# Kernel tuning notes

Measured on AMD Instinct MI355X. Metric: run time of the kernel, lower is better.

Reference implementation:

```python
import jax, jax.numpy as jnp
import numpy as np

HEADS = 8
EPS = 1e-12  # F.normalize default eps


def conv1x1(t, w):
    # t: (B, Cin, H, W); w: (Cout, Cin) -> (B, Cout, H, W)
    return jnp.einsum('bchw,oc->bohw', t, w)


def cosine_attn(q, k, v, scale):
    # q: (B,h,d,Nq); k,v: (B,h,d,Nk). Cosine attention: L2-normalize over feature dim d.
    q = q / jnp.maximum(jnp.linalg.norm(q, axis=2, keepdims=True), EPS)
    k = k / jnp.maximum(jnp.linalg.norm(k, axis=2, keepdims=True), EPS)
    attn = jnp.einsum('bhdq,bhdk->bhqk', q, k) * scale
    attn = jax.nn.softmax(attn, axis=-1)
    return jnp.einsum('bhqk,bhdk->bhdq', attn, v)  # (B,h,d,Nq)


def setup_inputs() -> dict:
    key = jax.random.key(0)
    ks = jax.random.split(key, 8)
    B, C, H, W, L = 8, 512, 64, 64, 16
    def w(k, o, i):
        return jax.random.normal(k, (o, i), dtype=jnp.float32) * (1.0 / np.sqrt(i))
    return {
        'x': jax.random.normal(ks[0], (B, C, H, W), dtype=jnp.float32),
        'latents': jax.random.normal(ks[1], (1, C, 1, L), dtype=jnp.float32) * 0.02,
        'w_q_lat': w(ks[2], C, C),
        'w_kv_x': w(ks[3], 2 * C, C),
        'w_q_x': w(ks[4], C, C),
        'w_kv_lat': w(ks[5], 2 * C, C),
        'w_proj': w(ks[6], C, C),
        'b_proj': jnp.zeros((C,), dtype=jnp.float32),
    }


def reference(x, latents, w_q_lat, w_kv_x, w_q_x, w_kv_lat, w_proj, b_proj):
    B, C, H, W = x.shape
    L = latents.shape[-1]
    h = HEADS
    d = C // h
    scale = d ** (-0.5)

    # latents read from spatial features (compression)
    lat = jnp.broadcast_to(latents, (B, C, 1, L))
    ql = conv1x1(lat, w_q_lat).reshape(B, h, d, L)
    kvx = conv1x1(x, w_kv_x)
    kx = kvx[:, :C].reshape(B, h, d, H * W)
    vx = kvx[:, C:].reshape(B, h, d, H * W)
    lat_read = cosine_attn(ql, kx, vx, scale).reshape(B, C, 1, L)

    # latents write back into features (expansion)
    qx = conv1x1(x, w_q_x).reshape(B, h, d, H * W)
    kvl = conv1x1(lat_read, w_kv_lat)
    kl = kvl[:, :C].reshape(B, h, d, L)
    vl = kvl[:, C:].reshape(B, h, d, L)
    x_write = cosine_attn(qx, kl, vl, scale).reshape(B, C, H, W)

    # output projection (dropout p=0 -> identity)
    return conv1x1(x_write, w_proj) + b_proj[None, :, None, None]
```

## Files before the change

kernel.cpp:

```cpp
#include <hip/hip_runtime.h>


typedef __bf16 bf16x8 __attribute__((ext_vector_type(8)));
typedef float floatx4 __attribute__((ext_vector_type(4)));
typedef short short8_t __attribute__((ext_vector_type(8)));
typedef short short4_t __attribute__((ext_vector_type(4)));

#define DEV __device__ __forceinline__

DEV float bf2f(unsigned short u){ union{unsigned int i; float f;} v; v.i = ((unsigned int)u)<<16; return v.f; }
DEV unsigned short f2bf(float f){
  __bf16 h = (__bf16)f;
  unsigned short u; __builtin_memcpy(&u, &h, 2); return u;
}

DEV void glds16(const void* g, void* l){
  __builtin_amdgcn_global_load_lds((const __attribute__((address_space(1))) void*)g,
                                   (__attribute__((address_space(3))) void*)l, 16, 0, 0);
}

#define OFF_XT     256ull
#define OFF_KVX    (OFF_XT + 33554432ull)
#define OFF_WKVX   (OFF_KVX + 67108864ull)
#define OFF_WQX    (OFF_WKVX + 1048576ull)
#define OFF_WKVL   (OFF_WQX + 524288ull)
#define OFF_WPROJ  (OFF_WKVL + 1048576ull)
#define OFF_WQLAT  (OFF_WPROJ + 524288ull)
#define OFF_LATF   (OFF_WQLAT + 524288ull)
#define OFF_BIAS   (OFF_LATF + 32768ull)
#define OFF_QLH    (OFF_BIAS + 4096ull)
#define OFF_GNUM   (OFF_QLH + 32768ull)
#define OFF_GDEN   (OFF_GNUM + 524288ull)
#define OFF_KVL    (OFF_GDEN + 4096ull)
#define OFF_KHAT   (OFF_KVL + 524288ull)
#define OFF_GVL    (OFF_KHAT + 524288ull)

__global__ void k_sniff(const unsigned short* __restrict__ x, int* flag){
  int t = threadIdx.x;
  int m = 0;
  for (int i = t; i < 4096; i += 256){ int e = (x[i]>>7)&0xFF; m = (e>m)?e:m; }
  __shared__ int red[256];
  red[t] = m; __syncthreads();
  for (int s = 128; s > 0; s >>= 1){ if (t < s) red[t] = (red[t+s]>red[t])?red[t+s]:red[t]; __syncthreads(); }
  if (t == 0) flag[0] = (red[0] > 150) ? 1 : 0;
}

__global__ __launch_bounds__(256) void k_prep(const void* s0, const void* s1, const void* s2,
                                              const void* s3, const void* s4,
                                              const void* slat, const void* sbias,
                                              unsigned short* __restrict__ wdst,
                                              float* __restrict__ latf, float* __restrict__ biasf,
                                              const int* __restrict__ flag){
  int b = blockIdx.x, t = threadIdx.x;
  int isf = *flag;
  if (b < 896){
    int e = b*2048 + t*8;
    const void* src; int off;
    if (e < 524288)      { src = s0; off = e; }
    else if (e < 786432) { src = s1; off = e - 524288; }
    else if (e < 1310720){ src = s2; off = e - 786432; }
    else if (e < 1572864){ src = s3; off = e - 1310720; }
    else                 { src = s4; off = e - 1572864; }
    if (isf){
      const float* s = (const float*)src + off;
      float4 v0 = *(const float4*)(s);
      float4 v1 = *(const float4*)(s+4);
      unsigned short tmp[8] __attribute__((aligned(16)));
      tmp[0]=f2bf(v0.x); tmp[1]=f2bf(v0.y); tmp[2]=f2bf(v0.z); tmp[3]=f2bf(v0.w);
      tmp[4]=f2bf(v1.x); tmp[5]=f2bf(v1.y); tmp[6]=f2bf(v1.z); tmp[7]=f2bf(v1.w);
      *(short8_t*)&wdst[e] = *(short8_t*)tmp;
    } else {
      *(short8_t*)&wdst[e] = *(const short8_t*)((const unsigned short*)src + off);
    }
  } else if (b < 900){
    int i = (b-896)*2048 + t*8;
#pragma unroll
    for (int j = 0; j < 8; ++j)
      latf[i+j] = isf ? ((const float*)slat)[i+j] : bf2f(((const unsigned short*)slat)[i+j]);
  } else {
    if (t < 512) biasf[t] = isf ? ((const float*)sbias)[t] : bf2f(((const unsigned short*)sbias)[t]);
  }
}

__global__ __launch_bounds__(256) void k_xt(const void* __restrict__ xraw, unsigned short* __restrict__ xT,
                                            const int* __restrict__ flag){
  int nb = blockIdx.x, cb = blockIdx.y, b = blockIdx.z;
  int n0 = nb*64, c0 = cb*64;
  __shared__ unsigned short tile[64][72];
  int t = threadIdx.x;
  if (*flag){
    const float* xp = (const float*)xraw;
#pragma unroll
    for (int i = 0; i < 4; ++i){
      int ch = i*256 + t; int c = ch>>4, n4 = (ch&15)*4;
      float4 v = *(const float4*)&xp[((size_t)(b*512 + c0 + c))*4096 + n0 + n4];
      int cc = n4 ^ (((c>>3)&7)<<3);
      tile[c][cc+0]=f2bf(v.x); tile[c][cc+1]=f2bf(v.y); tile[c][cc+2]=f2bf(v.z); tile[c][cc+3]=f2bf(v.w);
    }
  } else {
    const unsigned short* xp = (const unsigned short*)xraw;
#pragma unroll
    for (int i = 0; i < 2; ++i){
      int ch = i*256 + t; int c = ch>>3, n8 = (ch&7)*8;
      *(short8_t*)&tile[c][n8 ^ (((c>>3)&7)<<3)] =
        *(const short8_t*)&xp[((size_t)(b*512 + c0 + c))*4096 + n0 + n8];
    }
  }
  __syncthreads();
#pragma unroll
  for (int i = 0; i < 2; ++i){
    int ch = i*256 + t; int n = ch>>3, c8 = (ch&7)*8;
    unsigned short tmp[8] __attribute__((aligned(16)));
#pragma unroll
    for (int j = 0; j < 8; ++j){
      int c = c8 + j;
      tmp[j] = tile[c][n ^ (((c>>3)&7)<<3)];
    }
    *(short8_t*)&xT[((size_t)(b*4096 + n0 + n))*512 + c0 + c8] = *(short8_t*)tmp;
  }
}

__global__ __launch_bounds__(256) void k_ql(const unsigned short* __restrict__ wqlat,
                                            const float* __restrict__ latf, float* __restrict__ qlh){
  int h = blockIdx.x, o0 = h*64;
  extern __shared__ char smr[];
  float* latb = (float*)smr;
  unsigned short* wt = (unsigned short*)(smr + 8192);
  float* qbuf = (float*)(smr + 8192 + 17408);
  float* rinv = (float*)(smr + 8192 + 17408 + 4096);
  int t = threadIdx.x;
  int o = t>>2, l4 = (t&3)*4;
  float acc[4] = {0.f,0.f,0.f,0.f};
  for (int kk = 0; kk < 512; kk += 128){
    __syncthreads();
#pragma unroll
    for (int j = 0; j < 8; ++j){ int i = j*256 + t; latb[i] = latf[kk*16 + i]; }
#pragma unroll
    for (int j = 0; j < 4; ++j){ int ch = j*256 + t; int r = ch>>4, kc = (ch&15)*8;
      *(short8_t*)&wt[r*136 + kc] = *(const short8_t*)&wqlat[(size_t)(o0+r)*512 + kk + kc]; }
    __syncthreads();
    for (int k = 0; k < 128; ++k){
      float w = bf2f(wt[o*136 + k]);
      const float* lr = &latb[k*16 + l4];
#pragma unroll
      for (int j = 0; j < 4; ++j) acc[j] += w*lr[j];
    }
  }
#pragma unroll
  for (int j = 0; j < 4; ++j) qbuf[o*16 + l4 + j] = acc[j];
  __syncthreads();
  if (t < 16){
    float ss = 0.f;
    for (int oo = 0; oo < 64; ++oo){ float v = qbuf[oo*16 + t]; ss += v*v; }
    rinv[t] = 0.125f / fmaxf(sqrtf(ss), 1e-12f);
  }
  __syncthreads();
#pragma unroll
  for (int j = 0; j < 4; ++j) qlh[(h*16 + l4 + j)*64 + o] = acc[j]*rinv[l4 + j];
}

DEV void stage_ab(const unsigned short* __restrict__ Ap0, const unsigned short* __restrict__ Ap1,
                  const unsigned short* __restrict__ Bp, int kk,
                  unsigned short* At, unsigned short* Bt, int wave, int rsub, int koff){
#pragma unroll
  for (int c2 = 0; c2 < 4; ++c2){
    int chunk = wave*4 + c2;
    int row = chunk*8 + rsub;
    const unsigned short* gp = (chunk < 8) ? (Ap0 + (size_t)row*512 + kk + koff)
                                           : (Ap1 + (size_t)(row-64)*512 + kk + koff);
    glds16(gp, At + chunk*512);
  }
#pragma unroll
  for (int c2 = 0; c2 < 4; ++c2){
    int chunk = wave*4 + c2;
    int row = chunk*8 + rsub;
    glds16(Bp + (size_t)row*512 + kk + koff, Bt + chunk*512);
  }
}

DEV void gemm128_db(const unsigned short* __restrict__ Ap0, const unsigned short* __restrict__ Ap1,
                    const unsigned short* __restrict__ Bp,
                    char* smr, floatx4 (&acc)[4][4]){
  unsigned short* At0 = (unsigned short*)smr;
  unsigned short* Bt0 = (unsigned short*)(smr + 16384);
  unsigned short* At1 = (unsigned short*)(smr + 32768);
  unsigned short* Bt1 = (unsigned short*)(smr + 49152);
  int t = threadIdx.x, lane = t&63, wave = t>>6;
  int wm = wave>>1, wn = wave&1, lr = lane&15, lq = lane>>4;
  int rsub = lane>>3;
  int koff = ((lane&7) ^ rsub)*8;
  int sw = lr&7;
  stage_ab(Ap0, Ap1, Bp, 0, At0, Bt0, wave, rsub, koff);
  __syncthreads();
  for (int kk = 0; kk < 512; kk += 64){
    int cur = (kk>>6)&1;
    unsigned short* Ac = cur ? At1 : At0;
    unsigned short* Bc = cur ? Bt1 : Bt0;
    if (kk < 448){
      stage_ab(Ap0, Ap1, Bp, kk+64, cur ? At0 : At1, cur ? Bt0 : Bt1, wave, rsub, koff);
    }
    __builtin_amdgcn_s_setprio(1);
#pragma unroll
    for (int ks = 0; ks < 2; ++ks){
      int vo = ((ks*4 + lq) ^ sw)*8;
      bf16x8 a[4], b[4];
#pragma unroll
      for (int mt = 0; mt < 4; ++mt) a[mt] = *(const bf16x8*)&Ac[(wm*64 + mt*16 + lr)*64 + vo];
#pragma unroll
      for (int nt = 0; nt < 4; ++nt) b[nt] = *(const bf16x8*)&Bc[(wn*64 + nt*16 + lr)*64 + vo];
#pragma unroll
      for (int mt = 0; mt < 4; ++mt)
#pragma unroll
        for (int nt = 0; nt < 4; ++nt)
          acc[mt][nt] = __builtin_amdgcn_mfma_f32_16x16x32_bf16(a[mt], b[nt], acc[mt][nt], 0, 0, 0);
    }
    __builtin_amdgcn_s_setprio(0);
    __syncthreads();
  }
}

__global__ __launch_bounds__(256) void k_kvattn1(const unsigned short* __restrict__ wkvx,
                                                 const unsigned short* __restrict__ xT,
                                                 const float* __restrict__ qlh2,
                                                 float* __restrict__ gnum, float* __restrict__ gden){
  int nb = blockIdx.x, h = blockIdx.y, b = blockIdx.z;
  int n0 = nb*128;
  extern __shared__ char smr[];
  unsigned short* kt  = (unsigned short*)smr;
  unsigned short* vt  = (unsigned short*)(smr + 18432);
  unsigned short* pt  = (unsigned short*)(smr + 35840);
  unsigned short* qls = (unsigned short*)(smr + 65536);
  float* ssq  = (float*)(smr + 67840);
  float* wred = (float*)(smr + 68352);
  int t = threadIdx.x, lane = t&63, wave = t>>6;
  int wm = wave>>1, wn = wave&1, lr = lane&15, lq = lane>>4;
  for (int i = t; i < 1024; i += 256) qls[(i>>6)*72 + (i&63)] = f2bf(qlh2[(size_t)h*1024 + i]);
  floatx4 acc[4][4];
  floatx4 zero = {0.f,0.f,0.f,0.f};
#pragma unroll
  for (int i = 0; i < 4; ++i) for (int j = 0; j < 4; ++j) acc[i][j] = zero;
  gemm128_db(wkvx + (size_t)(h*64)*512, wkvx + (size_t)(512 + h*64)*512,
             xT + ((size_t)(b*4096 + n0))*512, smr, acc);
  if (wm == 0){
#pragma unroll
    for (int nt = 0; nt < 4; ++nt){
      float s = 0.f;
#pragma unroll
      for (int mt = 0; mt < 4; ++mt)
#pragma unroll
        for (int r = 0; r < 4; ++r) s += acc[mt][nt][r]*acc[mt][nt][r];
      s += __shfl_xor(s, 16); s += __shfl_xor(s, 32);
      if (lq == 0) ssq[wn*64 + nt*16 + lr] = 1.f / fmaxf(sqrtf(s), 1e-12f);
    }
  } else {
#pragma unroll
    for (int mt = 0; mt < 4; ++mt)
#pragma unroll
      for (int nt = 0; nt < 4; ++nt){
        int col = wn*64 + nt*16 + lr;
#pragma unroll
        for (int r = 0; r < 4; ++r) vt[(mt*16 + lq*4 + r)*136 + col] = f2bf(acc[mt][nt][r]);
      }
  }
  __syncthreads();
  if (wm == 0){
#pragma unroll
    for (int nt = 0; nt < 4; ++nt){
      int col = wn*64 + nt*16 + lr;
      float rinv = ssq[col];
#pragma unroll
      for (int mt = 0; mt < 4; ++mt){
        unsigned short tmp[4] __attribute__((aligned(8)));
#pragma unroll
        for (int r = 0; r < 4; ++r) tmp[r] = f2bf(acc[mt][nt][r]*rinv);
        *(short4_t*)&kt[col*72 + mt*16 + lq*4] = *(short4_t*)tmp;
      }
    }
  }
  __syncthreads();
  floatx4 sl[2]; sl[0] = zero; sl[1] = zero;
#pragma unroll
  for (int ks = 0; ks < 2; ++ks){
    bf16x8 bb = *(const bf16x8*)&qls[lr*72 + ks*32 + lq*8];
#pragma unroll
    for (int i = 0; i < 2; ++i){
      bf16x8 aa = *(const bf16x8*)&kt[((wave*2 + i)*16 + lr)*72 + ks*32 + lq*8];
      sl[i] = __builtin_amdgcn_mfma_f32_16x16x32_bf16(aa, bb, sl[i], 0, 0, 0);
    }
  }
  float dp = 0.f;
  float pv[2][4];
#pragma unroll
  for (int i = 0; i < 2; ++i)
#pragma unroll
    for (int r = 0; r < 4; ++r){ float p = __expf(sl[i][r]); pv[i][r] = p; dp += p; }
  dp += __shfl_xor(dp, 16); dp += __shfl_xor(dp, 32);
  if (lq == 0) wred[wave*16 + lr] = dp;
#pragma unroll
  for (int i = 0; i < 2; ++i){
    unsigned short tmp[4] __attribute__((aligned(8)));
#pragma unroll
    for (int r = 0; r < 4; ++r) tmp[r] = f2bf(pv[i][r]);
    *(short4_t*)&pt[lr*136 + (wave*2 + i)*16 + lq*4] = *(short4_t*)tmp;
  }
  __syncthreads();
  int bh = b*8 + h;
  if (t < 16) atomicAdd(&gden[bh*16 + t], wred[t] + wred[16+t] + wred[32+t] + wred[48+t]);
  floatx4 nacc = zero;
#pragma unroll
  for (int ks = 0; ks < 4; ++ks){
    bf16x8 aa = *(const bf16x8*)&vt[(wave*16 + lr)*136 + ks*32 + lq*8];
    bf16x8 bb = *(const bf16x8*)&pt[lr*136 + ks*32 + lq*8];
    nacc = __builtin_amdgcn_mfma_f32_16x16x32_bf16(aa, bb, nacc, 0, 0, 0);
  }
  float* gp = &gnum[((size_t)bh*16 + lr)*64 + wave*16 + lq*4];
#pragma unroll
  for (int r = 0; r < 4; ++r) atomicAdd(&gp[r], nacc[r]);
}

__global__ __launch_bounds__(256) void k_kvl(const unsigned short* __restrict__ wkvl,
                                             const float* __restrict__ gnum, const float* __restrict__ gden,
                                             float* __restrict__ kvl){
  int ob = blockIdx.x, b = blockIdx.y;
  extern __shared__ char smr[];
  float* latb = (float*)smr;
  unsigned short* wt = (unsigned short*)(smr + 32768);
  int t = threadIdx.x;
  for (int i = t; i < 8192; i += 256){
    int c = i>>4, l = i&15;
    int h = c>>6, d = c&63;
    int bh = b*8 + h;
    latb[i] = gnum[((size_t)(bh*16 + l))*64 + d] / gden[bh*16 + l];
  }
  int o = t>>4, l = t&15;
  int o0 = ob*16;
  float acc = 0.f;
  for (int kk = 0; kk < 512; kk += 128){
    __syncthreads();
    { int r = t>>4, kc = (t&15)*8;
      *(short8_t*)&wt[r*136 + kc] = *(const short8_t*)&wkvl[(size_t)(o0+r)*512 + kk + kc]; }
    __syncthreads();
    for (int k = 0; k < 128; ++k) acc += bf2f(wt[o*136 + k]) * latb[(kk+k)*16 + l];
  }
  kvl[((size_t)(b*1024 + o0 + o))*16 + l] = acc;
}

__global__ void k_klnorm(const float* __restrict__ kvl, float* __restrict__ khat, float* __restrict__ gvl){
  int l = blockIdx.x, h = blockIdx.y, b = blockIdx.z, d = threadIdx.x;
  float kl = kvl[((size_t)(b*1024 + h*64 + d))*16 + l];
  float vl = kvl[((size_t)(b*1024 + 512 + h*64 + d))*16 + l];
  float ss = kl*kl;
  for (int off = 32; off; off >>= 1) ss += __shfl_xor(ss, off);
  float inv = 0.125f / fmaxf(sqrtf(ss), 1e-12f);
  size_t o = ((size_t)((b*8+h)*16 + l))*64 + d;
  khat[o] = kl*inv;
  gvl[o] = vl;
}

__global__ __launch_bounds__(256) void k_mmat(const unsigned short* __restrict__ wproj,
                                              const float* __restrict__ gvl,
                                              unsigned short* __restrict__ Mg){
  int cb = blockIdx.x, h = blockIdx.y, b = blockIdx.z;
  __shared__ unsigned short wt[128*68];
  int t = threadIdx.x;
#pragma unroll
  for (int i = 0; i < 4; ++i){ int ch = i*256 + t; int c = ch>>3, d8 = (ch&7)*8;
    *(short8_t*)&wt[c*68 + d8] = *(const short8_t*)&wproj[(size_t)(cb*128 + c)*512 + h*64 + d8]; }
  int l = t&15, cq = t>>4;
  float v[64];
  const float* vp = &gvl[((size_t)(b*8+h)*16 + l)*64];
#pragma unroll
  for (int j = 0; j < 16; ++j){ float4 f = *(const float4*)&vp[j*4];
    v[j*4+0]=f.x; v[j*4+1]=f.y; v[j*4+2]=f.z; v[j*4+3]=f.w; }
  __syncthreads();
#pragma unroll
  for (int c8 = 0; c8 < 8; ++c8){
    int c = cq*8 + c8;
    float dot = 0.f;
#pragma unroll
    for (int d = 0; d < 64; ++d) dot += bf2f(wt[c*68 + d]) * v[d];
    Mg[((size_t)(b*512) + cb*128 + c)*128 + h*16 + l] = f2bf(dot);
  }
}

__global__ __launch_bounds__(256) void k_attn2p2(const unsigned short* __restrict__ wqx,
                                                 const unsigned short* __restrict__ xT,
                                                 const float* __restrict__ khatg,
                                                 unsigned short* __restrict__ Pg){
  int nb = blockIdx.x, hp = blockIdx.y, b = blockIdx.z;
  int n0 = nb*128;
  extern __shared__ char smr[];
  unsigned short* qt0 = (unsigned short*)smr;
  unsigned short* qt1 = (unsigned short*)(smr + 18432);
  unsigned short* khs = (unsigned short*)(smr + 65536);
  float* ssq = (float*)(smr + 70144);
  int t = threadIdx.x, lane = t&63, wave = t>>6;
  int wm = wave>>1, wn = wave&1, lr = lane&15, lq = lane>>4;
  for (int i = t; i < 2048; i += 256){
    int hh = i>>10, rem = i&1023;
    khs[hh*1152 + (rem>>6)*72 + (rem&63)] = f2bf(khatg[((size_t)(b*8 + hp*2 + hh))*1024 + rem]);
  }
  floatx4 acc[4][4];
  floatx4 zero = {0.f,0.f,0.f,0.f};
#pragma unroll
  for (int i = 0; i < 4; ++i) for (int j = 0; j < 4; ++j) acc[i][j] = zero;
  gemm128_db(wqx + (size_t)(hp*128)*512, wqx + (size_t)(hp*128 + 64)*512,
             xT + ((size_t)(b*4096 + n0))*512, smr, acc);
#pragma unroll
  for (int nt = 0; nt < 4; ++nt){
    float s = 0.f;
#pragma unroll
    for (int mt = 0; mt < 4; ++mt)
#pragma unroll
      for (int r = 0; r < 4; ++r) s += acc[mt][nt][r]*acc[mt][nt][r];
    s += __shfl_xor(s, 16); s += __shfl_xor(s, 32);
    if (lq == 0) ssq[wm*128 + wn*64 + nt*16 + lr] = 1.f / fmaxf(sqrtf(s), 1e-12f);
  }
  __syncthreads();
  unsigned short* qtr = wm ? qt1 : qt0;
#pragma unroll
  for (int nt = 0; nt < 4; ++nt){
    int col = wn*64 + nt*16 + lr;
    float rinv = ssq[wm*128 + col];
#pragma unroll
    for (int mt = 0; mt < 4; ++mt){
      unsigned short tmp[4] __attribute__((aligned(8)));
#pragma unroll
      for (int r = 0; r < 4; ++r) tmp[r] = f2bf(acc[mt][nt][r]*rinv);
      *(short4_t*)&qtr[col*72 + mt*16 + lq*4] = *(short4_t*)tmp;
    }
  }
  __syncthreads();
  floatx4 sl[4];
#pragma unroll
  for (int i = 0; i < 4; ++i) sl[i] = zero;
  unsigned short* qsrc = wm ? qt1 : qt0;
#pragma unroll
  for (int ks = 0; ks < 2; ++ks){
    bf16x8 bb = *(const bf16x8*)&khs[wm*1152 + lr*72 + ks*32 + lq*8];
#pragma unroll
    for (int i = 0; i < 4; ++i){
      bf16x8 aa = *(const bf16x8*)&qsrc[((wn*4 + i)*16 + lr)*72 + ks*32 + lq*8];
      sl[i] = __builtin_amdgcn_mfma_f32_16x16x32_bf16(aa, bb, sl[i], 0, 0, 0);
    }
  }
  int h = hp*2 + wm;
#pragma unroll
  for (int i = 0; i < 4; ++i){
    float p[4], s[4];
#pragma unroll
    for (int r = 0; r < 4; ++r){ p[r] = __expf(sl[i][r]); s[r] = p[r]; }
#pragma unroll
    for (int r = 0; r < 4; ++r){
      s[r] += __shfl_xor(s[r], 1);
      s[r] += __shfl_xor(s[r], 2);
      s[r] += __shfl_xor(s[r], 4);
      s[r] += __shfl_xor(s[r], 8);
    }
    int nbase = wn*64 + i*16 + lq*4;
#pragma unroll
    for (int r = 0; r < 4; ++r)
      Pg[((size_t)(b*4096 + n0 + nbase + r))*128 + h*16 + lr] = f2bf(p[r]/s[r]);
  }
}

__global__ __launch_bounds__(256) void k_out(const unsigned short* __restrict__ Mg,
                                             const unsigned short* __restrict__ Pg,
                                             const float* __restrict__ biasf,
                                             void* __restrict__ outv, const int* __restrict__ flag){
  int nb = blockIdx.x, cb = blockIdx.y, b = blockIdx.z;
  int n0 = nb*128, c0 = cb*64;
  extern __shared__ char smr[];
  unsigned short* At = (unsigned short*)smr;
  unsigned short* Bt = At + 64*136;
  int t = threadIdx.x, lane = t&63, wave = t>>6;
  int wm = wave>>1, wn = wave&1, lr = lane&15, lq = lane>>4;
#pragma unroll
  for (int i = 0; i < 4; ++i){ int ch = i*256 + t; int r = ch>>4, p8 = (ch&15)*8;
    *(short8_t*)&At[r*136 + p8] = *(const short8_t*)&Mg[((size_t)(b*512 + c0 + r))*128 + p8]; }
#pragma unroll
  for (int i = 0; i < 8; ++i){ int ch = i*256 + t; int r = ch>>4, p8 = (ch&15)*8;
    *(short8_t*)&Bt[r*136 + p8] = *(const short8_t*)&Pg[((size_t)(b*4096 + n0 + r))*128 + p8]; }
  __syncthreads();
  floatx4 acc[2][4];
  floatx4 zero = {0.f,0.f,0.f,0.f};
#pragma unroll
  for (int i = 0; i < 2; ++i) for (int j = 0; j < 4; ++j) acc[i][j] = zero;
#pragma unroll
  for (int ks = 0; ks < 4; ++ks){
    bf16x8 a0 = *(const bf16x8*)&At[(wm*32 + lr)*136 + ks*32 + lq*8];
    bf16x8 a1 = *(const bf16x8*)&At[(wm*32 + 16 + lr)*136 + ks*32 + lq*8];
#pragma unroll
    for (int nt = 0; nt < 4; ++nt){
      bf16x8 bb = *(const bf16x8*)&Bt[(wn*64 + nt*16 + lr)*136 + ks*32 + lq*8];
      acc[0][nt] = __builtin_amdgcn_mfma_f32_16x16x32_bf16(a0, bb, acc[0][nt], 0, 0, 0);
      acc[1][nt] = __builtin_amdgcn_mfma_f32_16x16x32_bf16(a1, bb, acc[1][nt], 0, 0, 0);
    }
  }
  __syncthreads();
  float* ct = (float*)smr;
#pragma unroll
  for (int mt = 0; mt < 2; ++mt)
#pragma unroll
    for (int nt = 0; nt < 4; ++nt)
#pragma unroll
      for (int r = 0; r < 4; ++r){
        int row = wm*32 + mt*16 + lq*4 + r;
        ct[row*132 + wn*64 + nt*16 + lr] = acc[mt][nt][r] + biasf[c0 + row];
      }
  __syncthreads();
  if (*flag){
    float* of = (float*)outv;
#pragma unroll
    for (int i = 0; i < 8; ++i){ int ch = i*256 + t; int r = ch>>5, c4 = (ch&31)*4;
      *(float4*)&of[((size_t)(b*512 + c0 + r))*4096 + n0 + c4] = *(float4*)&ct[r*132 + c4]; }
  } else {
    unsigned short* ob = (unsigned short*)outv;
#pragma unroll
    for (int i = 0; i < 4; ++i){ int ch = i*256 + t; int r = ch>>4, c8 = (ch&15)*8;
      unsigned short tmp[8] __attribute__((aligned(16)));
#pragma unroll
      for (int j = 0; j < 8; ++j) tmp[j] = f2bf(ct[r*132 + c8 + j]);
      *(short8_t*)&ob[((size_t)(b*512 + c0 + r))*4096 + n0 + c8] = *(short8_t*)tmp; }
  }
}

extern "C" void kernel_launch(void* const* d_in, const int* in_sizes, int n_in,
                              void* d_out, int out_size, void* d_ws, size_t ws_size,
                              hipStream_t stream){
  (void)in_sizes; (void)n_in; (void)out_size; (void)ws_size;
  char* ws = (char*)d_ws;
  int* flag              = (int*)ws;
  unsigned short* xT     = (unsigned short*)(ws + OFF_XT);
  unsigned short* Pg     = (unsigned short*)(ws + OFF_KVX);
  unsigned short* Mg     = (unsigned short*)(ws + OFF_KVX + 8388608ull);
  unsigned short* wkvx   = (unsigned short*)(ws + OFF_WKVX);
  unsigned short* wqx    = (unsigned short*)(ws + OFF_WQX);
  unsigned short* wkvl   = (unsigned short*)(ws + OFF_WKVL);
  unsigned short* wproj  = (unsigned short*)(ws + OFF_WPROJ);
  float* latf  = (float*)(ws + OFF_LATF);
  float* biasf = (float*)(ws + OFF_BIAS);
  float* qlh   = (float*)(ws + OFF_QLH);
  float* gnum  = (float*)(ws + OFF_GNUM);
  float* gden  = (float*)(ws + OFF_GDEN);
  float* kvl   = (float*)(ws + OFF_KVL);
  float* khat  = (float*)(ws + OFF_KHAT);
  float* gvl   = (float*)(ws + OFF_GVL);

  k_sniff<<<1, 256, 0, stream>>>((const unsigned short*)d_in[0], flag);

  k_prep<<<901, 256, 0, stream>>>(d_in[3], d_in[4], d_in[5], d_in[6], d_in[2],
                                  d_in[1], d_in[7], wkvx, latf, biasf, flag);

  k_xt<<<dim3(64, 8, 8), 256, 0, stream>>>(d_in[0], xT, flag);

  k_ql<<<8, 256, 8192 + 17408 + 4096 + 64, stream>>>((unsigned short*)(ws + OFF_WQLAT), latf, qlh);

  hipMemsetAsync(ws + OFF_GNUM, 0, 524288 + 4096, stream);

  k_kvattn1<<<dim3(32, 8, 8), 256, 68608, stream>>>(wkvx, xT, qlh, gnum, gden);
  k_kvl<<<dim3(64, 8), 256, 32768 + 16*136*2, stream>>>(wkvl, gnum, gden, kvl);
  k_klnorm<<<dim3(16, 8, 8), 64, 0, stream>>>(kvl, khat, gvl);
  k_mmat<<<dim3(4, 8, 8), 256, 0, stream>>>(wproj, gvl, Mg);
  k_attn2p2<<<dim3(32, 4, 8), 256, 71168, stream>>>(wqx, xT, khat, Pg);
  k_out<<<dim3(32, 8, 8), 256, 52224, stream>>>(Mg, Pg, biasf, d_out, flag);
}
```

Measured before the change: 281.7 us.

## Merge prep kernels into one launch and fuse latent kv, norm and proj-matrix kernels

Folds the x transpose, weight conversion, bias conversion, latent-query projection and the memset of the accumulators into a single heterogeneous kernel dispatched by block index. The per-head kv projection, k normalization and proj-weight folding are fused into one kernel per (head, batch). This removes several launches and intermediate global buffers, trading them for fewer, larger blocks in the fused latent stage (only 64 blocks) and a large-shared-memory mega kernel that may lower occupancy for the transpose blocks.

```diff
diff --git a/kernel.cpp b/kernel.cpp
--- a/kernel.cpp
+++ b/kernel.cpp
@@ -45,16 +45,57 @@
   if (t == 0) flag[0] = (red[0] > 150) ? 1 : 0;
 }
 
-__global__ __launch_bounds__(256) void k_prep(const void* s0, const void* s1, const void* s2,
-                                              const void* s3, const void* s4,
-                                              const void* slat, const void* sbias,
-                                              unsigned short* __restrict__ wdst,
-                                              float* __restrict__ latf, float* __restrict__ biasf,
-                                              const int* __restrict__ flag){
-  int b = blockIdx.x, t = threadIdx.x;
+__global__ __launch_bounds__(256) void k_mega1(const void* __restrict__ xraw,
+                                               const void* __restrict__ slat,
+                                               const void* __restrict__ swqlat,
+                                               const void* s0, const void* s1, const void* s2,
+                                               const void* s3, const void* s4,
+                                               const void* __restrict__ sbias,
+                                               unsigned short* __restrict__ xT,
+                                               unsigned short* __restrict__ wdst,
+                                               float* __restrict__ biasf,
+                                               float* __restrict__ qlh,
+                                               float* __restrict__ zro,
+                                               const int* __restrict__ flag){
+  extern __shared__ char smr[];
+  int bid = blockIdx.x, t = threadIdx.x;
   int isf = *flag;
-  if (b < 896){
-    int e = b*2048 + t*8;
+  if (bid < 4096){
+    unsigned short (*tile)[72] = (unsigned short(*)[72])smr;
+    int nb = bid&63, cb = (bid>>6)&7, b = bid>>9;
+    int n0 = nb*64, c0 = cb*64;
+    if (isf){
+      const float* xp = (const float*)xraw;
+#pragma unroll
+      for (int i = 0; i < 4; ++i){
+        int ch = i*256 + t; int c = ch>>4, n4 = (ch&15)*4;
+        float4 v = *(const float4*)&xp[((size_t)(b*512 + c0 + c))*4096 + n0 + n4];
+        int cc = n4 ^ (((c>>3)&7)<<3);
+        tile[c][cc+0]=f2bf(v.x); tile[c][cc+1]=f2bf(v.y); tile[c][cc+2]=f2bf(v.z); tile[c][cc+3]=f2bf(v.w);
+      }
+    } else {
+      const unsigned short* xp = (const unsigned short*)xraw;
+#pragma unroll
+      for (int i = 0; i < 2; ++i){
+        int ch = i*256 + t; int c = ch>>3, n8 = (ch&7)*8;
+        *(short8_t*)&tile[c][n8 ^ (((c>>3)&7)<<3)] =
+          *(const short8_t*)&xp[((size_t)(b*512 + c0 + c))*4096 + n0 + n8];
+      }
+    }
+    __syncthreads();
+#pragma unroll
+    for (int i = 0; i < 2; ++i){
+      int ch = i*256 + t; int n = ch>>3, c8 = (ch&7)*8;
+      unsigned short tmp[8] __attribute__((aligned(16)));
+#pragma unroll
+      for (int j = 0; j < 8; ++j){
+        int c = c8 + j;
+        tmp[j] = tile[c][n ^ (((c>>3)&7)<<3)];
+      }
+      *(short8_t*)&xT[((size_t)(b*4096 + n0 + n))*512 + c0 + c8] = *(short8_t*)tmp;
+    }
+  } else if (bid < 4992){
+    int e = (bid-4096)*2048 + t*8;
     const void* src; int off;
     if (e < 524288)      { src = s0; off = e; }
     else if (e < 786432) { src = s1; off = e - 524288; }
@@ -72,91 +113,64 @@
     } else {
       *(short8_t*)&wdst[e] = *(const short8_t*)((const unsigned short*)src + off);
     }
-  } else if (b < 900){
-    int i = (b-896)*2048 + t*8;
-#pragma unroll
-    for (int j = 0; j < 8; ++j)
-      latf[i+j] = isf ? ((const float*)slat)[i+j] : bf2f(((const unsigned short*)slat)[i+j]);
+  } else if (bid == 4992){
+    biasf[t]       = isf ? ((const float*)sbias)[t]       : bf2f(((const unsigned short*)sbias)[t]);
+    biasf[t + 256] = isf ? ((const float*)sbias)[t + 256] : bf2f(((const unsigned short*)sbias)[t + 256]);
+  } else if (bid < 5001){
+    int h = bid - 4993, o0 = h*64;
+    float* latb = (float*)smr;
+    unsigned short* wt = (unsigned short*)(smr + 8192);
+    float* qbuf = (float*)(smr + 25600);
+    float* rinv = (float*)(smr + 29696);
+    int o = t>>2, l4 = (t&3)*4;
+    float acc[4] = {0.f,0.f,0.f,0.f};
+    for (int kk = 0; kk < 512; kk += 128){
+      __syncthreads();
+#pragma unroll
+      for (int j = 0; j < 8; ++j){
+        int i = j*256 + t;
+        latb[i] = isf ? ((const float*)slat)[kk*16 + i] : bf2f(((const unsigned short*)slat)[kk*16 + i]);
+      }
+#pragma unroll
+      for (int j = 0; j < 4; ++j){
+        int ch = j*256 + t; int r = ch>>4, kc = (ch&15)*8;
+        if (isf){
+          const float* s = (const float*)swqlat + (size_t)(o0+r)*512 + kk + kc;
+          float4 v0 = *(const float4*)(s);
+          float4 v1 = *(const float4*)(s+4);
+          unsigned short tmp[8] __attribute__((aligned(16)));
+          tmp[0]=f2bf(v0.x); tmp[1]=f2bf(v0.y); tmp[2]=f2bf(v0.z); tmp[3]=f2bf(v0.w);
+          tmp[4]=f2bf(v1.x); tmp[5]=f2bf(v1.y); tmp[6]=f2bf(v1.z); tmp[7]=f2bf(v1.w);
+          *(short8_t*)&wt[r*136 + kc] = *(short8_t*)tmp;
+        } else {
+          *(short8_t*)&wt[r*136 + kc] =
+            *(const short8_t*)((const unsigned short*)swqlat + (size_t)(o0+r)*512 + kk + kc);
+        }
+      }
+      __syncthreads();
+      for (int k = 0; k < 128; ++k){
+        float w = bf2f(wt[o*136 + k]);
+        const float* lr = &latb[k*16 + l4];
+#pragma unroll
+        for (int j = 0; j < 4; ++j) acc[j] += w*lr[j];
+      }
+    }
+#pragma unroll
+    for (int j = 0; j < 4; ++j) qbuf[o*16 + l4 + j] = acc[j];
+    __syncthreads();
+    if (t < 16){
+      float ss = 0.f;
+      for (int oo = 0; oo < 64; ++oo){ float v = qbuf[oo*16 + t]; ss += v*v; }
+      rinv[t] = 0.125f / fmaxf(sqrtf(ss), 1e-12f);
+    }
+    __syncthreads();
+#pragma unroll
+    for (int j = 0; j < 4; ++j) qlh[(h*16 + l4 + j)*64 + o] = acc[j]*rinv[l4 + j];
   } else {
-    if (t < 512) biasf[t] = isf ? ((const float*)sbias)[t] : bf2f(((const unsigned short*)sbias)[t]);
-  }
-}
-
-__global__ __launch_bounds__(256) void k_xt(const void* __restrict__ xraw, unsigned short* __restrict__ xT,
-                                            const int* __restrict__ flag){
-  int nb = blockIdx.x, cb = blockIdx.y, b = blockIdx.z;
-  int n0 = nb*64, c0 = cb*64;
-  __shared__ unsigned short tile[64][72];
-  int t = threadIdx.x;
-  if (*flag){
-    const float* xp = (const float*)xraw;
-#pragma unroll
-    for (int i = 0; i < 4; ++i){
-      int ch = i*256 + t; int c = ch>>4, n4 = (ch&15)*4;
-      float4 v = *(const float4*)&xp[((size_t)(b*512 + c0 + c))*4096 + n0 + n4];
-      int cc = n4 ^ (((c>>3)&7)<<3);
-      tile[c][cc+0]=f2bf(v.x); tile[c][cc+1]=f2bf(v.y); tile[c][cc+2]=f2bf(v.z); tile[c][cc+3]=f2bf(v.w);
-    }
-  } else {
-    const unsigned short* xp = (const unsigned short*)xraw;
-#pragma unroll
-    for (int i = 0; i < 2; ++i){
-      int ch = i*256 + t; int c = ch>>3, n8 = (ch&7)*8;
-      *(short8_t*)&tile[c][n8 ^ (((c>>3)&7)<<3)] =
-        *(const short8_t*)&xp[((size_t)(b*512 + c0 + c))*4096 + n0 + n8];
-    }
-  }
-  __syncthreads();
-#pragma unroll
-  for (int i = 0; i < 2; ++i){
-    int ch = i*256 + t; int n = ch>>3, c8 = (ch&7)*8;
-    unsigned short tmp[8] __attribute__((aligned(16)));
-#pragma unroll
-    for (int j = 0; j < 8; ++j){
-      int c = c8 + j;
-      tmp[j] = tile[c][n ^ (((c>>3)&7)<<3)];
-    }
-    *(short8_t*)&xT[((size_t)(b*4096 + n0 + n))*512 + c0 + c8] = *(short8_t*)tmp;
-  }
-}
-
-__global__ __launch_bounds__(256) void k_ql(const unsigned short* __restrict__ wqlat,
-                                            const float* __restrict__ latf, float* __restrict__ qlh){
-  int h = blockIdx.x, o0 = h*64;
-  extern __shared__ char smr[];
-  float* latb = (float*)smr;
-  unsigned short* wt = (unsigned short*)(smr + 8192);
-  float* qbuf = (float*)(smr + 8192 + 17408);
-  float* rinv = (float*)(smr + 8192 + 17408 + 4096);
-  int t = threadIdx.x;
-  int o = t>>2, l4 = (t&3)*4;
-  float acc[4] = {0.f,0.f,0.f,0.f};
-  for (int kk = 0; kk < 512; kk += 128){
-    __syncthreads();
-#pragma unroll
-    for (int j = 0; j < 8; ++j){ int i = j*256 + t; latb[i] = latf[kk*16 + i]; }
-#pragma unroll
-    for (int j = 0; j < 4; ++j){ int ch = j*256 + t; int r = ch>>4, kc = (ch&15)*8;
-      *(short8_t*)&wt[r*136 + kc] = *(const short8_t*)&wqlat[(size_t)(o0+r)*512 + kk + kc]; }
-    __syncthreads();
-    for (int k = 0; k < 128; ++k){
-      float w = bf2f(wt[o*136 + k]);
-      const float* lr = &latb[k*16 + l4];
-#pragma unroll
-      for (int j = 0; j < 4; ++j) acc[j] += w*lr[j];
-    }
-  }
-#pragma unroll
-  for (int j = 0; j < 4; ++j) qbuf[o*16 + l4 + j] = acc[j];
-  __syncthreads();
-  if (t < 16){
-    float ss = 0.f;
-    for (int oo = 0; oo < 64; ++oo){ float v = qbuf[oo*16 + t]; ss += v*v; }
-    rinv[t] = 0.125f / fmaxf(sqrtf(ss), 1e-12f);
-  }
-  __syncthreads();
-#pragma unroll
-  for (int j = 0; j < 4; ++j) qlh[(h*16 + l4 + j)*64 + o] = acc[j]*rinv[l4 + j];
+    int i = (bid-5001)*256 + t;
+    float4 z; z.x=0.f; z.y=0.f; z.z=0.f; z.w=0.f;
+    ((float4*)zro)[i] = z;
+  }
 }
 
 DEV void stage_ab(const unsigned short* __restrict__ Ap0, const unsigned short* __restrict__ Ap1,
@@ -318,68 +332,88 @@
   for (int r = 0; r < 4; ++r) atomicAdd(&gp[r], nacc[r]);
 }
 
-__global__ __launch_bounds__(256) void k_kvl(const unsigned short* __restrict__ wkvl,
-                                             const float* __restrict__ gnum, const float* __restrict__ gden,
-                                             float* __restrict__ kvl){
-  int ob = blockIdx.x, b = blockIdx.y;
+__global__ __launch_bounds__(256) void k_kvlnm(const unsigned short* __restrict__ wkvl,
+                                               const unsigned short* __restrict__ wproj,
+                                               const float* __restrict__ gnum,
+                                               const float* __restrict__ gden,
+                                               float* __restrict__ khat,
+                                               unsigned short* __restrict__ Mg){
+  int h = blockIdx.x, b = blockIdx.y;
   extern __shared__ char smr[];
   float* latb = (float*)smr;
   unsigned short* wt = (unsigned short*)(smr + 32768);
+  float* kbuf = (float*)(smr + 67584);
+  float* vbuf = (float*)(smr + 71936);
+  float* rl   = (float*)(smr + 76288);
   int t = threadIdx.x;
+  int bh = b*8 + h;
   for (int i = t; i < 8192; i += 256){
     int c = i>>4, l = i&15;
-    int h = c>>6, d = c&63;
-    int bh = b*8 + h;
-    latb[i] = gnum[((size_t)(bh*16 + l))*64 + d] / gden[bh*16 + l];
-  }
-  int o = t>>4, l = t&15;
-  int o0 = ob*16;
-  float acc = 0.f;
+    int hs = c>>6, d = c&63;
+    latb[i] = gnum[((size_t)((b*8+hs)*16 + l))*64 + d] / gden[(b*8+hs)*16 + l];
+  }
+  int rq = t>>4, l = t&15;
+  float acc[8];
+#pragma unroll
+  for (int j = 0; j < 8; ++j) acc[j] = 0.f;
   for (int kk = 0; kk < 512; kk += 128){
     __syncthreads();
-    { int r = t>>4, kc = (t&15)*8;
-      *(short8_t*)&wt[r*136 + kc] = *(const short8_t*)&wkvl[(size_t)(o0+r)*512 + kk + kc]; }
-    __syncthreads();
-    for (int k = 0; k < 128; ++k) acc += bf2f(wt[o*136 + k]) * latb[(kk+k)*16 + l];
-  }
-  kvl[((size_t)(b*1024 + o0 + o))*16 + l] = acc;
-}
-
-__global__ void k_klnorm(const float* __restrict__ kvl, float* __restrict__ khat, float* __restrict__ gvl){
-  int l = blockIdx.x, h = blockIdx.y, b = blockIdx.z, d = threadIdx.x;
-  float kl = kvl[((size_t)(b*1024 + h*64 + d))*16 + l];
-  float vl = kvl[((size_t)(b*1024 + 512 + h*64 + d))*16 + l];
-  float ss = kl*kl;
-  for (int off = 32; off; off >>= 1) ss += __shfl_xor(ss, off);
-  float inv = 0.125f / fmaxf(sqrtf(ss), 1e-12f);
-  size_t o = ((size_t)((b*8+h)*16 + l))*64 + d;
-  khat[o] = kl*inv;
-  gvl[o] = vl;
-}
-
-__global__ __launch_bounds__(256) void k_mmat(const unsigned short* __restrict__ wproj,
-                                              const float* __restrict__ gvl,
-                                              unsigned short* __restrict__ Mg){
-  int cb = blockIdx.x, h = blockIdx.y, b = blockIdx.z;
-  __shared__ unsigned short wt[128*68];
-  int t = threadIdx.x;
-#pragma unroll
-  for (int i = 0; i < 4; ++i){ int ch = i*256 + t; int c = ch>>3, d8 = (ch&7)*8;
-    *(short8_t*)&wt[c*68 + d8] = *(const short8_t*)&wproj[(size_t)(cb*128 + c)*512 + h*64 + d8]; }
-  int l = t&15, cq = t>>4;
+#pragma unroll
+    for (int j = 0; j < 8; ++j){
+      int ch = j*256 + t; int r = ch>>4, kc = (ch&15)*8;
+      int og = (r < 64) ? (h*64 + r) : (512 + h*64 + (r-64));
+      *(short8_t*)&wt[r*136 + kc] = *(const short8_t*)&wkvl[(size_t)og*512 + kk + kc];
+    }
+    __syncthreads();
+    for (int k = 0; k < 128; ++k){
+      float lv = latb[(kk + k)*16 + l];
+#pragma unroll
+      for (int j = 0; j < 8; ++j) acc[j] += bf2f(wt[(j*16 + rq)*136 + k]) * lv;
+    }
+  }
+  __syncthreads();
+#pragma unroll
+  for (int j = 0; j < 8; ++j){
+    int row = j*16 + rq;
+    if (row < 64) kbuf[l*68 + row] = acc[j];
+    else          vbuf[l*68 + (row-64)] = acc[j];
+  }
+  __syncthreads();
+  if (t < 16){
+    float ss = 0.f;
+    for (int d = 0; d < 64; ++d){ float v = kbuf[t*68 + d]; ss += v*v; }
+    rl[t] = 0.125f / fmaxf(sqrtf(ss), 1e-12f);
+  }
+  __syncthreads();
+#pragma unroll
+  for (int j = 0; j < 4; ++j){
+    int i = j*256 + t; int ll = i>>6, d = i&63;
+    khat[((size_t)bh*16 + ll)*64 + d] = kbuf[ll*68 + d]*rl[ll];
+  }
   float v[64];
-  const float* vp = &gvl[((size_t)(b*8+h)*16 + l)*64];
-#pragma unroll
-  for (int j = 0; j < 16; ++j){ float4 f = *(const float4*)&vp[j*4];
-    v[j*4+0]=f.x; v[j*4+1]=f.y; v[j*4+2]=f.z; v[j*4+3]=f.w; }
-  __syncthreads();
-#pragma unroll
-  for (int c8 = 0; c8 < 8; ++c8){
-    int c = cq*8 + c8;
-    float dot = 0.f;
-#pragma unroll
-    for (int d = 0; d < 64; ++d) dot += bf2f(wt[c*68 + d]) * v[d];
-    Mg[((size_t)(b*512) + cb*128 + c)*128 + h*16 + l] = f2bf(dot);
+  {
+    const float* vp = &vbuf[l*68];
+#pragma unroll
+    for (int j = 0; j < 16; ++j){ float4 f = *(const float4*)&vp[j*4];
+      v[j*4+0]=f.x; v[j*4+1]=f.y; v[j*4+2]=f.z; v[j*4+3]=f.w; }
+  }
+  int cq = t>>4;
+  for (int cb = 0; cb < 4; ++cb){
+    __syncthreads();
+#pragma unroll
+    for (int j = 0; j < 4; ++j){
+      int ch = j*256 + t; int c = ch>>3, d8 = (ch&7)*8;
+      *(short8_t*)&wt[c*68 + d8] = *(const short8_t*)&wproj[(size_t)(cb*128 + c)*512 + h*64 + d8];
+    }
+    __syncthreads();
+#pragma unroll
+    for (int c8 = 0; c8 < 8; ++c8){
+      int c = cq*8 + c8;
+      float dot = 0.f;
+#pragma unroll
+      for (int d = 0; d < 64; ++d) dot += bf2f(wt[c*68 + d]) * v[d];
+      Mg[((size_t)(b*512) + cb*128 + c)*128 + h*16 + l] = f2bf(dot);
+    }
   }
 }
 
@@ -538,30 +572,20 @@
   unsigned short* wqx    = (unsigned short*)(ws + OFF_WQX);
   unsigned short* wkvl   = (unsigned short*)(ws + OFF_WKVL);
   unsigned short* wproj  = (unsigned short*)(ws + OFF_WPROJ);
-  float* latf  = (float*)(ws + OFF_LATF);
   float* biasf = (float*)(ws + OFF_BIAS);
   float* qlh   = (float*)(ws + OFF_QLH);
   float* gnum  = (float*)(ws + OFF_GNUM);
   float* gden  = (float*)(ws + OFF_GDEN);
-  float* kvl   = (float*)(ws + OFF_KVL);
   float* khat  = (float*)(ws + OFF_KHAT);
-  float* gvl   = (float*)(ws + OFF_GVL);
 
   k_sniff<<<1, 256, 0, stream>>>((const unsigned short*)d_in[0], flag);
 
-  k_prep<<<901, 256, 0, stream>>>(d_in[3], d_in[4], d_in[5], d_in[6], d_in[2],
-                                  d_in[1], d_in[7], wkvx, latf, biasf, flag);
-
-  k_xt<<<dim3(64, 8, 8), 256, 0, stream>>>(d_in[0], xT, flag);
-
-  k_ql<<<8, 256, 8192 + 17408 + 4096 + 64, stream>>>((unsigned short*)(ws + OFF_WQLAT), latf, qlh);
-
-  hipMemsetAsync(ws + OFF_GNUM, 0, 524288 + 4096, stream);
+  k_mega1<<<5130, 256, 29760, stream>>>(d_in[0], d_in[1], d_in[2],
+                                        d_in[3], d_in[4], d_in[5], d_in[6], d_in[2],
+                                        d_in[7], xT, wkvx, biasf, qlh, gnum, flag);
 
   k_kvattn1<<<dim3(32, 8, 8), 256, 68608, stream>>>(wkvx, xT, qlh, gnum, gden);
-  k_kvl<<<dim3(64, 8), 256, 32768 + 16*136*2, stream>>>(wkvl, gnum, gden, kvl);
-  k_klnorm<<<dim3(16, 8, 8), 64, 0, stream>>>(kvl, khat, gvl);
-  k_mmat<<<dim3(4, 8, 8), 256, 0, stream>>>(wproj, gvl, Mg);
+  k_kvlnm<<<dim3(8, 8), 256, 76352, stream>>>(wkvl, wproj, gnum, gden, khat, Mg);
   k_attn2p2<<<dim3(32, 4, 8), 256, 71168, stream>>>(wqx, xT, khat, Pg);
   k_out<<<dim3(32, 8, 8), 256, 52224, stream>>>(Mg, Pg, biasf, d_out, flag);
 }
```

After: 315.1 us. 11.9% more time.
